# Optimization experiments

Measured on AMD Instinct MI355X. Metric: run time of the kernel, lower is better.

Reference implementation:

```python
import jax, jax.numpy as jnp
import numpy as np

HIDDEN = 3584
N_HEADS = 16
N_KV = 8
HEAD_DIM = 256
INTER = 14336
EPS = 1e-6
SCALING = 256.0 ** -0.5  # query_pre_attn_scalar ** -0.5
SOFTCAP = 50.0
WINDOW = 1024
B, S = 2, 2048


def rmsnorm(x, w, eps=EPS):
    # Gemma2 style: scale by (1 + weight), weight zero-initialized
    var = jnp.mean(x * x, axis=-1, keepdims=True)
    return x * jax.lax.rsqrt(var + eps) * (1.0 + w)


def rotate_half(x):
    half = x.shape[-1] // 2
    return jnp.concatenate([-x[..., half:], x[..., :half]], axis=-1)


def setup_inputs() -> dict:
    key = jax.random.key(0)
    ks = jax.random.split(key, 12)
    hidden_states = jax.random.normal(ks[0], (B, S, HIDDEN), jnp.float32)
    # RoPE tables (theta = 10000)
    inv_freq = 1.0 / (10000.0 ** (np.arange(0, HEAD_DIM, 2, dtype=np.float32) / HEAD_DIM))
    t = np.arange(S, dtype=np.float32)
    freqs = np.outer(t, inv_freq)  # [S, HEAD_DIM/2]
    emb = np.concatenate([freqs, freqs], axis=-1)  # [S, HEAD_DIM]
    cos = jnp.asarray(np.cos(emb))
    sin = jnp.asarray(np.sin(emb))
    sd = lambda fan_in: 1.0 / np.sqrt(fan_in)
    Wq = jax.random.normal(ks[1], (N_HEADS * HEAD_DIM, HIDDEN), jnp.float32) * sd(HIDDEN)
    Wk = jax.random.normal(ks[2], (N_KV * HEAD_DIM, HIDDEN), jnp.float32) * sd(HIDDEN)
    Wv = jax.random.normal(ks[3], (N_KV * HEAD_DIM, HIDDEN), jnp.float32) * sd(HIDDEN)
    Wo = jax.random.normal(ks[4], (HIDDEN, N_HEADS * HEAD_DIM), jnp.float32) * sd(N_HEADS * HEAD_DIM)
    Wgate = jax.random.normal(ks[5], (INTER, HIDDEN), jnp.float32) * sd(HIDDEN)
    Wup = jax.random.normal(ks[6], (INTER, HIDDEN), jnp.float32) * sd(HIDDEN)
    Wdown = jax.random.normal(ks[7], (HIDDEN, INTER), jnp.float32) * sd(INTER)
    # RMSNorm weights zero-init per Gemma2 (effective scale 1.0), small perturbation
    w_in_ln = jax.random.normal(ks[8], (HIDDEN,), jnp.float32) * 0.02
    w_post_attn_ln = jax.random.normal(ks[9], (HIDDEN,), jnp.float32) * 0.02
    w_pre_ff_ln = jax.random.normal(ks[10], (HIDDEN,), jnp.float32) * 0.02
    w_post_ff_ln = jax.random.normal(ks[11], (HIDDEN,), jnp.float32) * 0.02
    return dict(hidden_states=hidden_states, cos=cos, sin=sin, Wq=Wq, Wk=Wk, Wv=Wv,
                Wo=Wo, Wgate=Wgate, Wup=Wup, Wdown=Wdown, w_in_ln=w_in_ln,
                w_post_attn_ln=w_post_attn_ln, w_pre_ff_ln=w_pre_ff_ln,
                w_post_ff_ln=w_post_ff_ln)


def _decoder_layer(hidden_states, cos, sin, Wq, Wk, Wv, Wo, Wgate, Wup, Wdown,
                   w_in_ln, w_post_attn_ln, w_pre_ff_ln, w_post_ff_ln):
    b, s, _ = hidden_states.shape
    residual = hidden_states
    x = rmsnorm(hidden_states, w_in_ln)

    # QKV projections (bias=False), bsnd layout
    q = jnp.einsum('bsh,oh->bso', x, Wq).reshape(b, s, N_HEADS, HEAD_DIM)
    k = jnp.einsum('bsh,oh->bso', x, Wk).reshape(b, s, N_KV, HEAD_DIM)
    v = jnp.einsum('bsh,oh->bso', x, Wv).reshape(b, s, N_KV, HEAD_DIM)

    # RoPE with explicit cos/sin, half-rotation; broadcast over batch & heads
    c = cos[None, :, None, :]
    sn = sin[None, :, None, :]
    q = q * c + rotate_half(q) * sn
    k = k * c + rotate_half(k) * sn

    # GQA: repeat KV heads
    rep = N_HEADS // N_KV
    k = jnp.repeat(k, rep, axis=2)  # [b, s, H, D]
    v = jnp.repeat(v, rep, axis=2)

    # scores with custom scaling + tanh softcap
    scores = jnp.einsum('bqhd,bkhd->bhqk', q, k) * SCALING
    scores = SOFTCAP * jnp.tanh(scores / SOFTCAP)

    # causal + sliding-window mask: attend to j with i-WINDOW < j <= i
    i = jnp.arange(s)[:, None]
    j = jnp.arange(s)[None, :]
    allowed = (j <= i) & (j > i - WINDOW)
    scores = jnp.where(allowed[None, None], scores, jnp.float32(-1e30))

    probs = jax.nn.softmax(scores, axis=-1)
    attn = jnp.einsum('bhqk,bkhd->bqhd', probs, v).reshape(b, s, N_HEADS * HEAD_DIM)
    attn = jnp.einsum('bso,ho->bsh', attn, Wo)

    hidden_states = residual + rmsnorm(attn, w_post_attn_ln)

    residual = hidden_states
    y = rmsnorm(hidden_states, w_pre_ff_ln)
    gate = jax.nn.gelu(jnp.einsum('bsh,ih->bsi', y, Wgate), approximate=True)
    up = jnp.einsum('bsh,ih->bsi', y, Wup)
    mlp = jnp.einsum('bsi,hi->bsh', gate * up, Wdown)
    hidden_states = residual + rmsnorm(mlp, w_post_ff_ln)
    return hidden_states


def reference(hidden_states, cos, sin, Wq, Wk, Wv, Wo, Wgate, Wup, Wdown,
              w_in_ln, w_post_attn_ln, w_pre_ff_ln, w_post_ff_ln):
    return _decoder_layer(hidden_states, cos, sin, Wq, Wk, Wv, Wo, Wgate, Wup,
                          Wdown, w_in_ln, w_post_attn_ln, w_pre_ff_ln, w_post_ff_ln)
```

## Files before the change

### kernel.cpp

```cpp
#include <hip/hip_runtime.h>
#include <hip/hip_bf16.h>

typedef __hip_bfloat16 bf16;
typedef __bf16 bf16x8_t __attribute__((ext_vector_type(8)));
typedef float f32x4_t __attribute__((ext_vector_type(4)));
typedef unsigned short u16x8_t __attribute__((ext_vector_type(8)));

#define HID 3584
#define SEQ 2048
#define NBATCH 2
#define MTOK 4096
#define NHEADS 16
#define NKVH 8
#define HDIM 256
#define QOUT 4096
#define KOUT 2048
#define INTERD 14336
#define EPSF 1e-6f

static __device__ __forceinline__ unsigned short f2bu(float f) {
  union { bf16 b; unsigned short u; } cv;
  cv.b = __float2bfloat16(f);
  return cv.u;
}

static __device__ __forceinline__ f32x4_t mfma16(bf16x8_t a, bf16x8_t b, f32x4_t c) {
  return __builtin_amdgcn_mfma_f32_16x16x32_bf16(a, b, c, 0, 0, 0);
}

static __device__ __forceinline__ void gl_lds16(const void* g, void* l) {
  __builtin_amdgcn_global_load_lds((__attribute__((address_space(1))) void*)g,
                                   (__attribute__((address_space(3))) void*)l,
                                   16, 0, 0);
}

static __device__ __forceinline__ float block_reduce_sum(float v) {
  __shared__ float buf[4];
  #pragma unroll
  for (int m = 1; m < 64; m <<= 1) v += __shfl_xor(v, m, 64);
  __syncthreads();
  if ((threadIdx.x & 63) == 0) buf[threadIdx.x >> 6] = v;
  __syncthreads();
  return buf[0] + buf[1] + buf[2] + buf[3];
}

__global__ __launch_bounds__(256) void cvt_w(
    const float* __restrict__ src, bf16* __restrict__ dst, int n) {
  const int stride = gridDim.x * 256 * 8;
  for (int i = (blockIdx.x * 256 + threadIdx.x) * 8; i < n; i += stride) {
    const float4 a = *(const float4*)(src + i);
    const float4 b = *(const float4*)(src + i + 4);
    u16x8_t o;
    o[0] = f2bu(a.x); o[1] = f2bu(a.y); o[2] = f2bu(a.z); o[3] = f2bu(a.w);
    o[4] = f2bu(b.x); o[5] = f2bu(b.y); o[6] = f2bu(b.z); o[7] = f2bu(b.w);
    *(u16x8_t*)(dst + i) = o;
  }
}

enum { EPI_BF16 = 0, EPI_F32 = 1, EPI_VT = 2, EPI_GELUMUL = 3, EPI_QKV = 4 };

template <int EPI>
__global__ __launch_bounds__(512, 2) void gemm8p(
    const bf16* __restrict__ A, const bf16* __restrict__ Bw,
    void* __restrict__ Cout, const bf16* __restrict__ aux,
    void* __restrict__ C2, void* __restrict__ C3,
    int Ndim, int Kdim) {
  __shared__ __align__(16) char L[131072];

  const int NT = Kdim >> 6;
  const int NB = gridDim.x;
  const int bid = blockIdx.x;
  const int sw = (bid & 7) * (NB >> 3) + (bid >> 3);
  const int m0 = (sw & 15) * 256;
  const int n0 = (sw >> 4) * 256;

  const int tid = threadIdx.x;
  const int wid = tid >> 6, l = tid & 63;
  const int wm = wid >> 2, wn = wid & 3;
  const int lr = l & 15, lg = l >> 4;

  const int rlane = wid * 16 + (l >> 3);
  const int lc8 = (((l & 7) ^ (l >> 3)) << 3);
  const bf16* srcA = A + (size_t)(m0 + rlane) * Kdim + lc8;
  const bf16* srcB = Bw + (size_t)(n0 + rlane) * Kdim + lc8;
  const size_t K128 = (size_t)Kdim << 7;
  const size_t K8 = (size_t)Kdim << 3;

  auto STAGE = [&](int op, int rh, int tl) {
    if (tl >= NT) return;
    const bf16* s = (op ? srcB : srcA) + (size_t)rh * K128 + ((size_t)tl << 6);
    char* d = L + ((tl & 1) << 16) + (op << 15) + (rh << 14) + (wid << 11);
    gl_lds16(s, d);
    gl_lds16(s + K8, d + 1024);
  };

  const int arow = wm * 128 + lr;
  const int brow = wn * 64 + lr;
  const int swz = lr & 7;
  const int csw0 = ((0 * 4 + lg) ^ swz) << 4;
  const int csw1 = ((1 * 4 + lg) ^ swz) << 4;
  auto LDA = [&](int mi, int kk, int c) {
    return *(const bf16x8_t*)(L + (c << 16) + arow * 128 + mi * 2048 +
                              (kk ? csw1 : csw0));
  };
  auto LDB = [&](int ni, int kk, int c) {
    return *(const bf16x8_t*)(L + (c << 16) + 32768 + brow * 128 + ni * 2048 +
                              (kk ? csw1 : csw0));
  };

  f32x4_t acc[8][4];
  #pragma unroll
  for (int i = 0; i < 8; i++)
    #pragma unroll
    for (int j = 0; j < 4; j++) acc[i][j] = (f32x4_t){0.f, 0.f, 0.f, 0.f};

  bf16x8_t fa[8][2], fb[4][2];

  STAGE(1, 0, 0); STAGE(1, 1, 0); STAGE(0, 0, 0); STAGE(0, 1, 0);
  STAGE(1, 0, 1); STAGE(1, 1, 1); STAGE(0, 0, 1); STAGE(0, 1, 1);
  asm volatile("s_waitcnt vmcnt(8)" ::: "memory");
  __builtin_amdgcn_s_barrier();
  __builtin_amdgcn_sched_barrier(0);

#define MFMA_Q(MB, NBQ)                                                        \
  _Pragma("unroll") for (int mi = 0; mi < 4; ++mi)                             \
  _Pragma("unroll") for (int ni = 0; ni < 2; ++ni) {                           \
    acc[MB + mi][NBQ + ni] =                                                   \
        mfma16(fa[MB + mi][0], fb[NBQ + ni][0], acc[MB + mi][NBQ + ni]);       \
    acc[MB + mi][NBQ + ni] =                                                   \
        mfma16(fa[MB + mi][1], fb[NBQ + ni][1], acc[MB + mi][NBQ + ni]);       \
  }

#define TILE(T, C)                                                             \
  {                                                                            \
                                \
    _Pragma("unroll") for (int mi = 0; mi < 4; ++mi) {                         \
      fa[mi][0] = LDA(mi, 0, (C)); fa[mi][1] = LDA(mi, 1, (C));                \
    }                                                                          \
    _Pragma("unroll") for (int ni = 0; ni < 2; ++ni) {                         \
      fb[ni][0] = LDB(ni, 0, (C)); fb[ni][1] = LDB(ni, 1, (C));                \
    }                                                                          \
    __builtin_amdgcn_s_barrier();                                              \
    asm volatile("s_waitcnt lgkmcnt(0)" ::: "memory");                         \
    __builtin_amdgcn_sched_barrier(0);                                         \
    __builtin_amdgcn_s_setprio(1);                                             \
    MFMA_Q(0, 0);                                                              \
    __builtin_amdgcn_s_setprio(0);                                             \
    __builtin_amdgcn_s_barrier();                                              \
    __builtin_amdgcn_sched_barrier(0);                                         \
                                        \
    _Pragma("unroll") for (int ni = 2; ni < 4; ++ni) {                         \
      fb[ni][0] = LDB(ni, 0, (C)); fb[ni][1] = LDB(ni, 1, (C));                \
    }                                                                          \
    __builtin_amdgcn_s_barrier();                                              \
    asm volatile("s_waitcnt lgkmcnt(0)" ::: "memory");                         \
    __builtin_amdgcn_sched_barrier(0);                                         \
    __builtin_amdgcn_s_setprio(1);                                             \
    MFMA_Q(0, 2);                                                              \
    __builtin_amdgcn_s_setprio(0);                                             \
    __builtin_amdgcn_s_barrier();                                              \
    __builtin_amdgcn_sched_barrier(0);                                         \
                     \
    _Pragma("unroll") for (int mi = 4; mi < 8; ++mi) {                         \
      fa[mi][0] = LDA(mi, 0, (C)); fa[mi][1] = LDA(mi, 1, (C));                \
    }                                                                          \
    STAGE(1, 0, (T) + 2);                                                      \
    STAGE(1, 1, (T) + 2);                                                      \
    __builtin_amdgcn_s_barrier();                                              \
    asm volatile("s_waitcnt lgkmcnt(0)" ::: "memory");                         \
    __builtin_amdgcn_sched_barrier(0);                                         \
    __builtin_amdgcn_s_setprio(1);                                             \
    MFMA_Q(4, 0);                                                              \
    __builtin_amdgcn_s_setprio(0);                                             \
    __builtin_amdgcn_s_barrier();                                              \
    __builtin_amdgcn_sched_barrier(0);                                         \
             \
    STAGE(0, 0, (T) + 2);                                                      \
    STAGE(0, 1, (T) + 2);                                                      \
    __builtin_amdgcn_s_barrier();                                              \
    __builtin_amdgcn_s_setprio(1);                                             \
    MFMA_Q(4, 2);                                                              \
    __builtin_amdgcn_s_setprio(0);                                             \
    if ((T) + 2 < NT) {                                                        \
      asm volatile("s_waitcnt vmcnt(8)" ::: "memory");                         \
    } else {                                                                   \
      asm volatile("s_waitcnt vmcnt(0)" ::: "memory");                         \
    }                                                                          \
    __builtin_amdgcn_s_barrier();                                              \
    __builtin_amdgcn_sched_barrier(0);                                         \
  }

  for (int t = 0; t < NT; t += 2) {
    TILE(t, 0);
    TILE(t + 1, 1);
  }
#undef TILE
#undef MFMA_Q

  const int row0 = m0 + wm * 128 + lg * 4;
  const int col0 = n0 + wn * 64 + lr;
  #pragma unroll
  for (int mi = 0; mi < 8; mi++) {
    #pragma unroll
    for (int ni = 0; ni < 4; ni++) {
      #pragma unroll
      for (int r = 0; r < 4; r++) {
        const int row = row0 + mi * 16 + r;
        const int col = col0 + ni * 16;
        const float v = acc[mi][ni][r];
        if constexpr (EPI == EPI_BF16) {
          ((bf16*)Cout)[(size_t)row * Ndim + col] = __float2bfloat16(v);
        } else if constexpr (EPI == EPI_F32) {
          ((float*)Cout)[(size_t)row * Ndim + col] = v;
        } else if constexpr (EPI == EPI_VT) {
          const int kvh = col >> 8, d = col & 255;
          const int bb = row >> 11, s = row & 2047;
          ((bf16*)Cout)[(((size_t)((bb * 8 + kvh) * 256 + d)) << 11) + s] =
              __float2bfloat16(v);
        } else if constexpr (EPI == EPI_QKV) {
          if (col < 4096) {
            ((bf16*)Cout)[(size_t)row * 4096 + col] = __float2bfloat16(v);
          } else if (col < 6144) {
            ((bf16*)C2)[(size_t)row * 2048 + (col - 4096)] =
                __float2bfloat16(v);
          } else {
            const int cc = col - 6144;
            const int kvh = cc >> 8, d = cc & 255;
            const int bb = row >> 11, s = row & 2047;
            ((bf16*)C3)[(((size_t)((bb * 8 + kvh) * 256 + d)) << 11) + s] =
                __float2bfloat16(v);
          }
        } else {
          const float g = __bfloat162float(aux[(size_t)row * Ndim + col]);
          const float u = 0.7978845608028654f * (g + 0.044715f * g * g * g);
          const float gl = 0.5f * g * (1.f + tanhf(u));
          ((bf16*)Cout)[(size_t)row * Ndim + col] = __float2bfloat16(gl * v);
        }
      }
    }
  }
  (void)aux; (void)C2; (void)C3;
}

__global__ __launch_bounds__(256) void rmsnorm_in(
    const float* __restrict__ x, const float* __restrict__ w,
    bf16* __restrict__ out) {
  const int row = blockIdx.x, t = threadIdx.x;
  const float4* xr = (const float4*)(x + (size_t)row * HID);
  float4 v[4];
  float ss = 0.f;
  #pragma unroll
  for (int j = 0; j < 4; j++) {
    const int idx = t + 256 * j;
    if (idx < HID / 4) {
      v[j] = xr[idx];
      ss += v[j].x * v[j].x + v[j].y * v[j].y + v[j].z * v[j].z + v[j].w * v[j].w;
    }
  }
  ss = block_reduce_sum(ss);
  const float sc = rsqrtf(ss * (1.f / HID) + EPSF);
  const float4* w4 = (const float4*)w;
  bf16* orow = out + (size_t)row * HID;
  #pragma unroll
  for (int j = 0; j < 4; j++) {
    const int idx = t + 256 * j;
    if (idx < HID / 4) {
      const float4 wv = w4[idx];
      ushort4 o;
      o.x = f2bu(v[j].x * sc * (1.f + wv.x));
      o.y = f2bu(v[j].y * sc * (1.f + wv.y));
      o.z = f2bu(v[j].z * sc * (1.f + wv.z));
      o.w = f2bu(v[j].w * sc * (1.f + wv.w));
      *(ushort4*)(orow + idx * 4) = o;
    }
  }
}

__global__ __launch_bounds__(128) void rope_kernel(
    bf16* __restrict__ q, bf16* __restrict__ k,
    const float* __restrict__ cosb, const float* __restrict__ sinb) {
  const int tok = blockIdx.x;
  const int hs = blockIdx.y;
  const int d = threadIdx.x;
  const int s = tok & (SEQ - 1);
  bf16* ptr = (hs < NHEADS)
                  ? q + (size_t)tok * QOUT + hs * HDIM
                  : k + (size_t)tok * KOUT + (hs - NHEADS) * HDIM;
  const float c = cosb[s * HDIM + d];
  const float sn = sinb[s * HDIM + d];
  const float x0 = __bfloat162float(ptr[d]);
  const float x1 = __bfloat162float(ptr[d + 128]);
  ptr[d] = __float2bfloat16(x0 * c - x1 * sn);
  ptr[d + 128] = __float2bfloat16(x1 * c + x0 * sn);
}

__global__ __launch_bounds__(256) void attn_kernel(
    const bf16* __restrict__ q, const bf16* __restrict__ k,
    const bf16* __restrict__ vt, bf16* __restrict__ out) {
  __shared__ __align__(16) bf16 plds[4][16 * 32];

  const int qt = blockIdx.x, h = blockIdx.y, b = blockIdx.z;
  const int w = threadIdx.x >> 6, l = threadIdx.x & 63;
  const int kvh = h >> 1;
  const int qbase = qt * 64 + w * 16;
  const int lr = l & 15, lg = l >> 4, lk = lg * 8;

  bf16x8_t qf[8];
  const bf16* qrow = q + (size_t)(b * SEQ + qbase + lr) * QOUT + h * HDIM;
  #pragma unroll
  for (int c = 0; c < 8; c++) qf[c] = *(const bf16x8_t*)(qrow + c * 32 + lk);

  f32x4_t acc[16];
  #pragma unroll
  for (int i = 0; i < 16; i++) acc[i] = (f32x4_t){0.f, 0.f, 0.f, 0.f};
  float L[4] = {0.f, 0.f, 0.f, 0.f};

  const bf16* kp = k + (size_t)(b * SEQ) * KOUT + kvh * HDIM;
  const bf16* vp = vt + (size_t)(b * NKVH + kvh) * HDIM * SEQ;
  bf16* pl = &plds[w][0];

  int kstart = qbase - 1023;
  if (kstart < 0) kstart = 0;
  kstart &= ~31;
  const int kend = qbase + 15;

  for (int kb = kstart; kb <= kend; kb += 32) {
    f32x4_t s0 = (f32x4_t){0.f, 0.f, 0.f, 0.f};
    f32x4_t s1 = (f32x4_t){0.f, 0.f, 0.f, 0.f};
    #pragma unroll
    for (int c = 0; c < 8; c++) {
      bf16x8_t k0 = *(const bf16x8_t*)(kp + (size_t)(kb + lr) * KOUT + c * 32 + lk);
      bf16x8_t k1 = *(const bf16x8_t*)(kp + (size_t)(kb + 16 + lr) * KOUT + c * 32 + lk);
      s0 = mfma16(qf[c], k0, s0);
      s1 = mfma16(qf[c], k1, s1);
    }
    float p[8];
    #pragma unroll
    for (int sub = 0; sub < 2; sub++) {
      const int j = kb + sub * 16 + lr;
      #pragma unroll
      for (int r = 0; r < 4; r++) {
        const int i = qbase + lg * 4 + r;
        float sc = (sub ? s1[r] : s0[r]) * 0.0625f;
        sc = 50.f * tanhf(sc * 0.02f);
        const bool ok = (j <= i) && (j > i - 1024);
        p[sub * 4 + r] = ok ? __expf(sc) : 0.f;
      }
    }
    #pragma unroll
    for (int r = 0; r < 4; r++) {
      float ps = p[r] + p[4 + r];
      ps += __shfl_xor(ps, 1, 64);
      ps += __shfl_xor(ps, 2, 64);
      ps += __shfl_xor(ps, 4, 64);
      ps += __shfl_xor(ps, 8, 64);
      L[r] += ps;
    }
    #pragma unroll
    for (int sub = 0; sub < 2; sub++)
      #pragma unroll
      for (int r = 0; r < 4; r++)
        pl[(lg * 4 + r) * 32 + sub * 16 + lr] = __float2bfloat16(p[sub * 4 + r]);
    asm volatile("s_waitcnt lgkmcnt(0)" ::: "memory");
    const bf16x8_t pa = *(const bf16x8_t*)(pl + lr * 32 + lk);
    #pragma unroll
    for (int dt = 0; dt < 16; dt++) {
      bf16x8_t bv = *(const bf16x8_t*)(vp + (size_t)(dt * 16 + lr) * SEQ + kb + lk);
      acc[dt] = mfma16(pa, bv, acc[dt]);
    }
  }

  float rL[4];
  #pragma unroll
  for (int r = 0; r < 4; r++) rL[r] = 1.f / L[r];
  #pragma unroll
  for (int dt = 0; dt < 16; dt++) {
    #pragma unroll
    for (int r = 0; r < 4; r++) {
      const int tok = b * SEQ + qbase + lg * 4 + r;
      out[(size_t)tok * QOUT + h * HDIM + dt * 16 + lr] =
          __float2bfloat16(acc[dt][r] * rL[r]);
    }
  }
}

__global__ __launch_bounds__(256) void fuse_attn(
    const float* __restrict__ hidden, const float* __restrict__ ap,
    const float* __restrict__ w_post, const float* __restrict__ w_pre,
    float* __restrict__ h1, bf16* __restrict__ y) {
  const int row = blockIdx.x, t = threadIdx.x;
  const float4* ar = (const float4*)(ap + (size_t)row * HID);
  const float4* hr = (const float4*)(hidden + (size_t)row * HID);
  float4 a[4];
  float ss = 0.f;
  #pragma unroll
  for (int j = 0; j < 4; j++) {
    const int idx = t + 256 * j;
    if (idx < HID / 4) {
      a[j] = ar[idx];
      ss += a[j].x * a[j].x + a[j].y * a[j].y + a[j].z * a[j].z + a[j].w * a[j].w;
    }
  }
  ss = block_reduce_sum(ss);
  const float sc = rsqrtf(ss * (1.f / HID) + EPSF);
  const float4* wpo = (const float4*)w_post;
  float4* h1r = (float4*)(h1 + (size_t)row * HID);
  float4 hv[4];
  float ss2 = 0.f;
  #pragma unroll
  for (int j = 0; j < 4; j++) {
    const int idx = t + 256 * j;
    if (idx < HID / 4) {
      const float4 wv = wpo[idx];
      const float4 x = hr[idx];
      hv[j].x = x.x + a[j].x * sc * (1.f + wv.x);
      hv[j].y = x.y + a[j].y * sc * (1.f + wv.y);
      hv[j].z = x.z + a[j].z * sc * (1.f + wv.z);
      hv[j].w = x.w + a[j].w * sc * (1.f + wv.w);
      ss2 += hv[j].x * hv[j].x + hv[j].y * hv[j].y + hv[j].z * hv[j].z + hv[j].w * hv[j].w;
      h1r[idx] = hv[j];
    }
  }
  ss2 = block_reduce_sum(ss2);
  const float sc2 = rsqrtf(ss2 * (1.f / HID) + EPSF);
  const float4* wpr = (const float4*)w_pre;
  bf16* yr = y + (size_t)row * HID;
  #pragma unroll
  for (int j = 0; j < 4; j++) {
    const int idx = t + 256 * j;
    if (idx < HID / 4) {
      const float4 wv = wpr[idx];
      ushort4 o;
      o.x = f2bu(hv[j].x * sc2 * (1.f + wv.x));
      o.y = f2bu(hv[j].y * sc2 * (1.f + wv.y));
      o.z = f2bu(hv[j].z * sc2 * (1.f + wv.z));
      o.w = f2bu(hv[j].w * sc2 * (1.f + wv.w));
      *(ushort4*)(yr + idx * 4) = o;
    }
  }
}

__global__ __launch_bounds__(256) void fuse_out(
    const float* __restrict__ h1, const float* __restrict__ mlp,
    const float* __restrict__ w, float* __restrict__ out) {
  const int row = blockIdx.x, t = threadIdx.x;
  const float4* mr = (const float4*)(mlp + (size_t)row * HID);
  float4 m[4];
  float ss = 0.f;
  #pragma unroll
  for (int j = 0; j < 4; j++) {
    const int idx = t + 256 * j;
    if (idx < HID / 4) {
      m[j] = mr[idx];
      ss += m[j].x * m[j].x + m[j].y * m[j].y + m[j].z * m[j].z + m[j].w * m[j].w;
    }
  }
  ss = block_reduce_sum(ss);
  const float sc = rsqrtf(ss * (1.f / HID) + EPSF);
  const float4* hr = (const float4*)(h1 + (size_t)row * HID);
  const float4* w4 = (const float4*)w;
  float4* orow = (float4*)(out + (size_t)row * HID);
  #pragma unroll
  for (int j = 0; j < 4; j++) {
    const int idx = t + 256 * j;
    if (idx < HID / 4) {
      const float4 wv = w4[idx];
      const float4 x = hr[idx];
      float4 o;
      o.x = x.x + m[j].x * sc * (1.f + wv.x);
      o.y = x.y + m[j].y * sc * (1.f + wv.y);
      o.z = x.z + m[j].z * sc * (1.f + wv.z);
      o.w = x.w + m[j].w * sc * (1.f + wv.w);
      orow[idx] = o;
    }
  }
}

extern "C" void kernel_launch(void* const* d_in, const int* in_sizes, int n_in,
                              void* d_out, int out_size, void* d_ws,
                              size_t ws_size, hipStream_t stream) {
  const float* hidden = (const float*)d_in[0];
  const float* cosb = (const float*)d_in[1];
  const float* sinb = (const float*)d_in[2];
  const float* Wq = (const float*)d_in[3];
  const float* Wk = (const float*)d_in[4];
  const float* Wv = (const float*)d_in[5];
  const float* Wo = (const float*)d_in[6];
  const float* Wgate = (const float*)d_in[7];
  const float* Wup = (const float*)d_in[8];
  const float* Wdown = (const float*)d_in[9];
  const float* w_in = (const float*)d_in[10];
  const float* w_post_attn = (const float*)d_in[11];
  const float* w_pre_ff = (const float*)d_in[12];
  const float* w_post_ff = (const float*)d_in[13];
  float* out = (float*)d_out;

  (void)in_sizes; (void)n_in; (void)out_size; (void)ws_size;

  const size_t WB = 102760448;
  char* ws = (char*)d_ws;
  bf16* wbuf = (bf16*)ws;
  char* ab = ws + WB;

  bf16* xn = (bf16*)(ab);
  bf16* q = (bf16*)(ab + 29360128);
  float* attn_proj = (float*)(ab);
  float* mlp = (float*)(ab);
  bf16* kbuf = (bf16*)(ab + 62914560);
  bf16* vt = (bf16*)(ab + 62914560 + 16777216);
  bf16* attn_out = (bf16*)(ab + 62914560 + 33554432);
  float* h1 = (float*)(ab + 62914560);
  bf16* y = (bf16*)(ab + 130023424);
  bf16* gate = (bf16*)(ab + 159383552);

  rmsnorm_in<<<MTOK, 256, 0, stream>>>(hidden, w_in, xn);

  cvt_w<<<4096, 256, 0, stream>>>(Wq, wbuf, QOUT * HID);
  cvt_w<<<2048, 256, 0, stream>>>(Wk, wbuf + (size_t)QOUT * HID, KOUT * HID);
  cvt_w<<<2048, 256, 0, stream>>>(Wv, wbuf + (size_t)(QOUT + KOUT) * HID,
                                  KOUT * HID);
  gemm8p<EPI_QKV><<<(8192 / 256) * 16, 512, 0, stream>>>(
      xn, wbuf, q, nullptr, kbuf, vt, 8192, HID);
  rope_kernel<<<dim3(MTOK, NHEADS + NKVH), 128, 0, stream>>>(q, kbuf, cosb, sinb);
  attn_kernel<<<dim3(SEQ / 64, NHEADS, NBATCH), 256, 0, stream>>>(
      q, kbuf, vt, attn_out);
  cvt_w<<<4096, 256, 0, stream>>>(Wo, wbuf, HID * QOUT);
  gemm8p<EPI_F32><<<(HID / 256) * 16, 512, 0, stream>>>(
      attn_out, wbuf, attn_proj, nullptr, nullptr, nullptr, HID, QOUT);
  fuse_attn<<<MTOK, 256, 0, stream>>>(hidden, attn_proj, w_post_attn,
                                      w_pre_ff, h1, y);
  cvt_w<<<4096, 256, 0, stream>>>(Wgate, wbuf, INTERD * HID);
  gemm8p<EPI_BF16><<<(INTERD / 256) * 16, 512, 0, stream>>>(
      y, wbuf, gate, nullptr, nullptr, nullptr, INTERD, HID);
  cvt_w<<<4096, 256, 0, stream>>>(Wup, wbuf, INTERD * HID);
  gemm8p<EPI_GELUMUL><<<(INTERD / 256) * 16, 512, 0, stream>>>(
      y, wbuf, gate, gate, nullptr, nullptr, INTERD, HID);
  cvt_w<<<4096, 256, 0, stream>>>(Wdown, wbuf, HID * INTERD);
  gemm8p<EPI_F32><<<(HID / 256) * 16, 512, 0, stream>>>(
      gate, wbuf, mlp, nullptr, nullptr, nullptr, HID, INTERD);

  fuse_out<<<MTOK, 256, 0, stream>>>(h1, mlp, w_post_ff, out);
}
```

Measured before the change: 2.787 ms.

## Trim GEMM main-loop barriers and compute V transposed via swapped-operand GEMM

Removes several s_barrier and sched_barrier calls inside the GEMM tile loop and issues the next B-tile global-to-LDS stages before the second-half A fragment loads, so waves stall less on synchronization. The V projection is split out of the fused QKV GEMM and computed as Wv·xnᵀ, so the epilogue writes the transposed V layout with contiguous sequence-index stores instead of the old strided scatter. A runtime mshift parameter replaces the hard-coded tile-index mapping so grids with 8 M-tiles work. Fewer barriers risk LDS read/write races between waves, and the extra launch adds a small cost.

```diff
diff --git a/kernel.cpp b/kernel.cpp
--- a/kernel.cpp
+++ b/kernel.cpp
@@ -57,22 +57,21 @@
   }
 }
 
-enum { EPI_BF16 = 0, EPI_F32 = 1, EPI_VT = 2, EPI_GELUMUL = 3, EPI_QKV = 4 };
+enum { EPI_BF16 = 0, EPI_F32 = 1, EPI_GELUMUL = 2, EPI_QK = 3, EPI_VSW = 4 };
 
 template <int EPI>
 __global__ __launch_bounds__(512, 2) void gemm8p(
     const bf16* __restrict__ A, const bf16* __restrict__ Bw,
     void* __restrict__ Cout, const bf16* __restrict__ aux,
-    void* __restrict__ C2, void* __restrict__ C3,
-    int Ndim, int Kdim) {
+    void* __restrict__ C2, int Ndim, int Kdim, int mshift) {
   __shared__ __align__(16) char L[131072];
 
   const int NT = Kdim >> 6;
   const int NB = gridDim.x;
   const int bid = blockIdx.x;
   const int sw = (bid & 7) * (NB >> 3) + (bid >> 3);
-  const int m0 = (sw & 15) * 256;
-  const int n0 = (sw >> 4) * 256;
+  const int m0 = (sw & ((1 << mshift) - 1)) << 8;
+  const int n0 = (sw >> mshift) << 8;
 
   const int tid = threadIdx.x;
   const int wid = tid >> 6, l = tid & 63;
@@ -133,51 +132,46 @@
 
 #define TILE(T, C)                                                             \
   {                                                                            \
-                                \
+                \
     _Pragma("unroll") for (int mi = 0; mi < 4; ++mi) {                         \
       fa[mi][0] = LDA(mi, 0, (C)); fa[mi][1] = LDA(mi, 1, (C));                \
     }                                                                          \
     _Pragma("unroll") for (int ni = 0; ni < 2; ++ni) {                         \
       fb[ni][0] = LDB(ni, 0, (C)); fb[ni][1] = LDB(ni, 1, (C));                \
     }                                                                          \
-    __builtin_amdgcn_s_barrier();                                              \
     asm volatile("s_waitcnt lgkmcnt(0)" ::: "memory");                         \
     __builtin_amdgcn_sched_barrier(0);                                         \
     __builtin_amdgcn_s_setprio(1);                                             \
     MFMA_Q(0, 0);                                                              \
     __builtin_amdgcn_s_setprio(0);                                             \
     __builtin_amdgcn_s_barrier();                                              \
-    __builtin_amdgcn_sched_barrier(0);                                         \
-                                        \
+      \
     _Pragma("unroll") for (int ni = 2; ni < 4; ++ni) {                         \
       fb[ni][0] = LDB(ni, 0, (C)); fb[ni][1] = LDB(ni, 1, (C));                \
     }                                                                          \
-    __builtin_amdgcn_s_barrier();                                              \
     asm volatile("s_waitcnt lgkmcnt(0)" ::: "memory");                         \
     __builtin_amdgcn_sched_barrier(0);                                         \
     __builtin_amdgcn_s_setprio(1);                                             \
     MFMA_Q(0, 2);                                                              \
     __builtin_amdgcn_s_setprio(0);                                             \
     __builtin_amdgcn_s_barrier();                                              \
-    __builtin_amdgcn_sched_barrier(0);                                         \
-                     \
+     \
+                                         \
+    STAGE(1, 0, (T) + 2);                                                      \
+    STAGE(1, 1, (T) + 2);                                                      \
     _Pragma("unroll") for (int mi = 4; mi < 8; ++mi) {                         \
       fa[mi][0] = LDA(mi, 0, (C)); fa[mi][1] = LDA(mi, 1, (C));                \
     }                                                                          \
-    STAGE(1, 0, (T) + 2);                                                      \
-    STAGE(1, 1, (T) + 2);                                                      \
-    __builtin_amdgcn_s_barrier();                                              \
     asm volatile("s_waitcnt lgkmcnt(0)" ::: "memory");                         \
     __builtin_amdgcn_sched_barrier(0);                                         \
     __builtin_amdgcn_s_setprio(1);                                             \
     MFMA_Q(4, 0);                                                              \
     __builtin_amdgcn_s_setprio(0);                                             \
     __builtin_amdgcn_s_barrier();                                              \
-    __builtin_amdgcn_sched_barrier(0);                                         \
-             \
+    \
+                    \
     STAGE(0, 0, (T) + 2);                                                      \
     STAGE(0, 1, (T) + 2);                                                      \
-    __builtin_amdgcn_s_barrier();                                              \
     __builtin_amdgcn_s_setprio(1);                                             \
     MFMA_Q(4, 2);                                                              \
     __builtin_amdgcn_s_setprio(0);                                             \
@@ -212,24 +206,17 @@
           ((bf16*)Cout)[(size_t)row * Ndim + col] = __float2bfloat16(v);
         } else if constexpr (EPI == EPI_F32) {
           ((float*)Cout)[(size_t)row * Ndim + col] = v;
-        } else if constexpr (EPI == EPI_VT) {
-          const int kvh = col >> 8, d = col & 255;
-          const int bb = row >> 11, s = row & 2047;
-          ((bf16*)Cout)[(((size_t)((bb * 8 + kvh) * 256 + d)) << 11) + s] =
-              __float2bfloat16(v);
-        } else if constexpr (EPI == EPI_QKV) {
+        } else if constexpr (EPI == EPI_QK) {
           if (col < 4096) {
             ((bf16*)Cout)[(size_t)row * 4096 + col] = __float2bfloat16(v);
-          } else if (col < 6144) {
+          } else {
             ((bf16*)C2)[(size_t)row * 2048 + (col - 4096)] =
                 __float2bfloat16(v);
-          } else {
-            const int cc = col - 6144;
-            const int kvh = cc >> 8, d = cc & 255;
-            const int bb = row >> 11, s = row & 2047;
-            ((bf16*)C3)[(((size_t)((bb * 8 + kvh) * 256 + d)) << 11) + s] =
-                __float2bfloat16(v);
           }
+        } else if constexpr (EPI == EPI_VSW) {
+          const int bb = col >> 11, s = col & 2047;
+          ((bf16*)Cout)[(((size_t)((bb * 8 + (row >> 8)) * 256 + (row & 255)))
+                         << 11) + s] = __float2bfloat16(v);
         } else {
           const float g = __bfloat162float(aux[(size_t)row * Ndim + col]);
           const float u = 0.7978845608028654f * (g + 0.044715f * g * g * g);
@@ -239,7 +226,7 @@
       }
     }
   }
-  (void)aux; (void)C2; (void)C3;
+  (void)aux; (void)C2;
 }
 
 __global__ __launch_bounds__(256) void rmsnorm_in(
@@ -519,25 +506,28 @@
   cvt_w<<<2048, 256, 0, stream>>>(Wk, wbuf + (size_t)QOUT * HID, KOUT * HID);
   cvt_w<<<2048, 256, 0, stream>>>(Wv, wbuf + (size_t)(QOUT + KOUT) * HID,
                                   KOUT * HID);
-  gemm8p<EPI_QKV><<<(8192 / 256) * 16, 512, 0, stream>>>(
-      xn, wbuf, q, nullptr, kbuf, vt, 8192, HID);
+  gemm8p<EPI_QK><<<(6144 / 256) * 16, 512, 0, stream>>>(
+      xn, wbuf, q, nullptr, kbuf, 6144, HID, 4);
+  gemm8p<EPI_VSW><<<(4096 / 256) * 8, 512, 0, stream>>>(
+      wbuf + (size_t)(QOUT + KOUT) * HID, xn, vt, nullptr, nullptr,
+      4096, HID, 3);
   rope_kernel<<<dim3(MTOK, NHEADS + NKVH), 128, 0, stream>>>(q, kbuf, cosb, sinb);
   attn_kernel<<<dim3(SEQ / 64, NHEADS, NBATCH), 256, 0, stream>>>(
       q, kbuf, vt, attn_out);
   cvt_w<<<4096, 256, 0, stream>>>(Wo, wbuf, HID * QOUT);
   gemm8p<EPI_F32><<<(HID / 256) * 16, 512, 0, stream>>>(
-      attn_out, wbuf, attn_proj, nullptr, nullptr, nullptr, HID, QOUT);
+      attn_out, wbuf, attn_proj, nullptr, nullptr, HID, QOUT, 4);
   fuse_attn<<<MTOK, 256, 0, stream>>>(hidden, attn_proj, w_post_attn,
                                       w_pre_ff, h1, y);
   cvt_w<<<4096, 256, 0, stream>>>(Wgate, wbuf, INTERD * HID);
   gemm8p<EPI_BF16><<<(INTERD / 256) * 16, 512, 0, stream>>>(
-      y, wbuf, gate, nullptr, nullptr, nullptr, INTERD, HID);
+      y, wbuf, gate, nullptr, nullptr, INTERD, HID, 4);
   cvt_w<<<4096, 256, 0, stream>>>(Wup, wbuf, INTERD * HID);
   gemm8p<EPI_GELUMUL><<<(INTERD / 256) * 16, 512, 0, stream>>>(
-      y, wbuf, gate, gate, nullptr, nullptr, INTERD, HID);
+      y, wbuf, gate, gate, nullptr, INTERD, HID, 4);
   cvt_w<<<4096, 256, 0, stream>>>(Wdown, wbuf, HID * INTERD);
   gemm8p<EPI_F32><<<(HID / 256) * 16, 512, 0, stream>>>(
-      gate, wbuf, mlp, nullptr, nullptr, nullptr, HID, INTERD);
+      gate, wbuf, mlp, nullptr, nullptr, HID, INTERD, 4);
 
   fuse_out<<<MTOK, 256, 0, stream>>>(h1, mlp, w_post_ff, out);
 }
```

Result: no change. 2.735 ms (-1.9%).
